# Kernel optimization log

Measured on AMD Instinct MI355X. Metric: run time of the kernel, lower is better.

## Reference

```python
import jax, jax.numpy as jnp
import numpy as np

M, N = 24, 12
H1 = (M + N) * 10 * 8        # 2880
HID = (M * M + N * N) * 10   # 7200
H2 = M * N * 4               # 1152
DOUT = M * N                 # 288
EPS = 1e-12


def setup_inputs() -> dict:
    key = jax.random.key(0)
    ks = jax.random.split(key, 16)
    s = 0.02  # weight scale
    return {
        "yt": jax.random.normal(ks[0], (N,), jnp.float32),
        "F": jax.random.normal(ks[1], (M, M), jnp.float32) * 0.1,
        "Hm": jax.random.normal(ks[2], (N, M), jnp.float32) * 0.1,
        "m1x_posterior": jax.random.normal(ks[3], (M, 1), jnp.float32),
        "m1x_prior_old": jax.random.normal(ks[4], (M, 1), jnp.float32),
        "hn": jax.random.normal(ks[5], (HID,), jnp.float32),
        "W1": jax.random.normal(ks[6], (H1, M + N), jnp.float32) * s,
        "b1": jax.random.normal(ks[7], (H1,), jnp.float32) * s,
        "Wih": jax.random.normal(ks[8], (3 * HID, H1), jnp.float32) * s,
        "Whh": jax.random.normal(ks[9], (3 * HID, HID), jnp.float32) * s,
        "bih": jax.random.normal(ks[10], (3 * HID,), jnp.float32) * s,
        "bhh": jax.random.normal(ks[11], (3 * HID,), jnp.float32) * s,
        "W2": jax.random.normal(ks[12], (H2, HID), jnp.float32) * s,
        "b2": jax.random.normal(ks[13], (H2,), jnp.float32) * s,
        "W3": jax.random.normal(ks[14], (DOUT, H2), jnp.float32) * s,
        "b3": jax.random.normal(ks[15], (DOUT,), jnp.float32) * s,
    }


def _l2_normalize(x):
    # torch F.normalize(p=2, dim=0, eps=1e-12)
    return x / jnp.maximum(jnp.linalg.norm(x), EPS)


def _gru_cell(x, h, Wih, Whh, bih, bhh):
    gi = Wih @ x + bih            # [3*HID]
    gh = Whh @ h + bhh            # [3*HID]
    gi_r, gi_z, gi_n = jnp.split(gi, 3)
    gh_r, gh_z, gh_n = jnp.split(gh, 3)
    r = jax.nn.sigmoid(gi_r + gh_r)
    z = jax.nn.sigmoid(gi_z + gh_z)
    n = jnp.tanh(gi_n + r * gh_n)
    return (1.0 - z) * n + z * h


def reference(yt, F, Hm, m1x_posterior, m1x_prior_old, hn,
              W1, b1, Wih, Whh, bih, bhh, W2, b2, W3, b3):
    # step_prior
    m1x_prior = F @ m1x_posterior        # [M,1]
    m1y = Hm @ m1x_prior                 # [N,1]
    # step_KGain_est
    dm1x = _l2_normalize((m1x_posterior - m1x_prior_old)[:, 0])  # [M]
    dm1y = _l2_normalize(yt - m1y[:, 0])                         # [N]
    kg_in = jnp.concatenate([dm1y, dm1x])                        # [M+N]
    l1 = jax.nn.relu(W1 @ kg_in + b1)                            # [H1]
    h_new = _gru_cell(l1, hn, Wih, Whh, bih, bhh)                # [HID]
    l2 = jax.nn.relu(W2 @ h_new + b2)                            # [H2]
    kg = (W3 @ l2 + b3).reshape(M, N)                            # Kalman gain
    # KNet_step update
    dy = yt[:, None] - m1y                                       # [N,1]
    m1x_post_new = m1x_prior + kg @ dy                           # [M,1]
    return m1x_post_new[:, 0]
```

## Files before the change

kernel.cpp:

```cpp
#include <hip/hip_runtime.h>
#include <math.h>

#define M_DIM 24
#define N_DIM 12
#define H1    2880
#define HID   7200
#define H2    1152
#define DOUT  288

#define WS_PRIOR 0
#define WS_KGIN  32
#define WS_DY    96
#define WS_L1    128
#define WS_HNEW  3072
#define WS_L2    10304
#define WS_KG    11520

__device__ __forceinline__ float wave_sum(float v) {
    #pragma unroll
    for (int o = 32; o; o >>= 1) v += __shfl_xor(v, o);
    return v;
}

__global__ void k_head(const float* __restrict__ yt, const float* __restrict__ F,
                       const float* __restrict__ Hm, const float* __restrict__ post,
                       const float* __restrict__ prior_old, float* __restrict__ ws) {
    __shared__ float s_prior[M_DIM];
    __shared__ float s_m1y[N_DIM];
    int t = threadIdx.x;
    if (t < M_DIM) {
        float acc = 0.f;
        #pragma unroll
        for (int j = 0; j < M_DIM; ++j) acc += F[t * M_DIM + j] * post[j];
        s_prior[t] = acc;
    }
    __syncthreads();
    if (t < N_DIM) {
        float acc = 0.f;
        #pragma unroll
        for (int j = 0; j < M_DIM; ++j) acc += Hm[t * M_DIM + j] * s_prior[j];
        s_m1y[t] = acc;
    }
    __syncthreads();
    float vx = 0.f;
    if (t < M_DIM) vx = post[t] - prior_old[t];
    float nx = fmaxf(sqrtf(wave_sum(vx * vx)), 1e-12f);
    float vy = 0.f;
    if (t < N_DIM) vy = yt[t] - s_m1y[t];
    float ny = fmaxf(sqrtf(wave_sum(vy * vy)), 1e-12f);
    if (t < N_DIM) ws[WS_KGIN + t] = vy / ny;
    if (t < M_DIM) ws[WS_KGIN + N_DIM + t] = vx / nx;
    if (t < M_DIM) ws[WS_PRIOR + t] = s_prior[t];
    if (t < N_DIM) ws[WS_DY + t] = vy;
}

__global__ __launch_bounds__(256) void k_l1(const float* __restrict__ W1,
                                            const float* __restrict__ b1,
                                            float* __restrict__ ws) {
    __shared__ float s_x[M_DIM + N_DIM];
    int t = threadIdx.x, lane = t & 63, w = t >> 6;
    if (t < M_DIM + N_DIM) s_x[t] = ws[WS_KGIN + t];
    __syncthreads();
    int i = blockIdx.x * 4 + w;
    float acc = (lane < M_DIM + N_DIM)
              ? W1[(size_t)i * (M_DIM + N_DIM) + lane] * s_x[lane] : 0.f;
    acc = wave_sum(acc);
    if (lane == 0) ws[WS_L1 + i] = fmaxf(acc + b1[i], 0.f);
}

__global__ __launch_bounds__(256) void k_gru(const float* __restrict__ Wih,
                                             const float* __restrict__ Whh,
                                             const float* __restrict__ bih,
                                             const float* __restrict__ bhh,
                                             const float* __restrict__ hn,
                                             float* __restrict__ ws) {
    __shared__ float s_l1[H1];
    __shared__ float s_h[HID];
    int t = threadIdx.x;
    float4* s_l14 = (float4*)s_l1;
    float4* s_h4  = (float4*)s_h;
    const float4* l14 = (const float4*)(ws + WS_L1);
    const float4* h4  = (const float4*)hn;
    for (int k = t; k < H1 / 4; k += 256)  s_l14[k] = l14[k];
    for (int k = t; k < HID / 4; k += 256) s_h4[k]  = h4[k];
    __syncthreads();

    int lane = t & 63, w = t >> 6;
    int i = blockIdx.x * 4 + w;

    const float4* wr = (const float4*)(Wih + (size_t)i * H1);
    const float4* wz = (const float4*)(Wih + (size_t)(i + HID) * H1);
    const float4* wn = (const float4*)(Wih + (size_t)(i + 2 * HID) * H1);
    float ar = 0.f, az = 0.f, an = 0.f;
    for (int k = lane; k < H1 / 4; k += 64) {
        float4 x = s_l14[k];
        float4 a = wr[k], b = wz[k], c = wn[k];
        ar += a.x * x.x + a.y * x.y + a.z * x.z + a.w * x.w;
        az += b.x * x.x + b.y * x.y + b.z * x.z + b.w * x.w;
        an += c.x * x.x + c.y * x.y + c.z * x.z + c.w * x.w;
    }

    const float4* ur = (const float4*)(Whh + (size_t)i * HID);
    const float4* uz = (const float4*)(Whh + (size_t)(i + HID) * HID);
    const float4* un = (const float4*)(Whh + (size_t)(i + 2 * HID) * HID);
    float hr = 0.f, hz = 0.f, hh = 0.f;
    for (int k = lane; k < HID / 4; k += 64) {
        float4 x = s_h4[k];
        float4 a = ur[k], b = uz[k], c = un[k];
        hr += a.x * x.x + a.y * x.y + a.z * x.z + a.w * x.w;
        hz += b.x * x.x + b.y * x.y + b.z * x.z + b.w * x.w;
        hh += c.x * x.x + c.y * x.y + c.z * x.z + c.w * x.w;
    }

    ar = wave_sum(ar); az = wave_sum(az); an = wave_sum(an);
    hr = wave_sum(hr); hz = wave_sum(hz); hh = wave_sum(hh);

    if (lane == 0) {
        float gr = ar + bih[i] + hr + bhh[i];
        float gz = az + bih[i + HID] + hz + bhh[i + HID];
        float r = 1.f / (1.f + expf(-gr));
        float z = 1.f / (1.f + expf(-gz));
        float n = tanhf(an + bih[i + 2 * HID] + r * (hh + bhh[i + 2 * HID]));
        ws[WS_HNEW + i] = (1.f - z) * n + z * s_h[i];
    }
}

__global__ __launch_bounds__(256) void k_l2(const float* __restrict__ W2,
                                            const float* __restrict__ b2,
                                            float* __restrict__ ws) {
    __shared__ float s_h[HID];
    int t = threadIdx.x;
    float4* s_h4 = (float4*)s_h;
    const float4* h4 = (const float4*)(ws + WS_HNEW);
    for (int k = t; k < HID / 4; k += 256) s_h4[k] = h4[k];
    __syncthreads();
    int lane = t & 63, w = t >> 6;
    int i = blockIdx.x * 4 + w;
    const float4* wr = (const float4*)(W2 + (size_t)i * HID);
    float acc = 0.f;
    for (int k = lane; k < HID / 4; k += 64) {
        float4 x = s_h4[k];
        float4 a = wr[k];
        acc += a.x * x.x + a.y * x.y + a.z * x.z + a.w * x.w;
    }
    acc = wave_sum(acc);
    if (lane == 0) ws[WS_L2 + i] = fmaxf(acc + b2[i], 0.f);
}

__global__ __launch_bounds__(256) void k_kg(const float* __restrict__ W3,
                                            const float* __restrict__ b3,
                                            float* __restrict__ ws) {
    __shared__ float s_x[H2];
    int t = threadIdx.x;
    float4* s_x4 = (float4*)s_x;
    const float4* x4 = (const float4*)(ws + WS_L2);
    for (int k = t; k < H2 / 4; k += 256) s_x4[k] = x4[k];
    __syncthreads();
    int lane = t & 63, w = t >> 6;
    int i = blockIdx.x * 4 + w;
    const float4* wr = (const float4*)(W3 + (size_t)i * H2);
    float acc = 0.f;
    for (int k = lane; k < H2 / 4; k += 64) {
        float4 x = s_x4[k];
        float4 a = wr[k];
        acc += a.x * x.x + a.y * x.y + a.z * x.z + a.w * x.w;
    }
    acc = wave_sum(acc);
    if (lane == 0) ws[WS_KG + i] = acc + b3[i];
}

__global__ void k_out(const float* __restrict__ ws, float* __restrict__ out) {
    int t = threadIdx.x;
    if (t < M_DIM) {
        float acc = ws[WS_PRIOR + t];
        #pragma unroll
        for (int n = 0; n < N_DIM; ++n)
            acc += ws[WS_KG + t * N_DIM + n] * ws[WS_DY + n];
        out[t] = acc;
    }
}

extern "C" void kernel_launch(void* const* d_in, const int* in_sizes, int n_in,
                              void* d_out, int out_size, void* d_ws, size_t ws_size,
                              hipStream_t stream) {
    const float* yt        = (const float*)d_in[0];
    const float* F         = (const float*)d_in[1];
    const float* Hm        = (const float*)d_in[2];
    const float* post      = (const float*)d_in[3];
    const float* prior_old = (const float*)d_in[4];
    const float* hn        = (const float*)d_in[5];
    const float* W1        = (const float*)d_in[6];
    const float* b1        = (const float*)d_in[7];
    const float* Wih       = (const float*)d_in[8];
    const float* Whh       = (const float*)d_in[9];
    const float* bih       = (const float*)d_in[10];
    const float* bhh       = (const float*)d_in[11];
    const float* W2        = (const float*)d_in[12];
    const float* b2        = (const float*)d_in[13];
    const float* W3        = (const float*)d_in[14];
    const float* b3        = (const float*)d_in[15];
    float* out = (float*)d_out;
    float* ws  = (float*)d_ws;

    k_head<<<1, 64, 0, stream>>>(yt, F, Hm, post, prior_old, ws);
    k_l1 <<<H1 / 4, 256, 0, stream>>>(W1, b1, ws);
    k_gru<<<HID / 4, 256, 0, stream>>>(Wih, Whh, bih, bhh, hn, ws);
    k_l2 <<<H2 / 4, 256, 0, stream>>>(W2, b2, ws);
    k_kg <<<DOUT / 4, 256, 0, stream>>>(W3, b3, ws);
    k_out<<<1, 64, 0, stream>>>(ws, out);
}
```

Measured before the change: 193.3 us.

## Fuse head into L1 and KG into output; drop shared-memory staging in GEMVs

The prior/normalization head is now recomputed redundantly in every L1 block, and the Kalman-gain GEMV is fused with the final update so each block produces one output row. This cuts the launch count from six to four. The GRU and L2 kernels no longer stage the input vector into shared memory; they read it straight from global memory, which should be served from cache. Those kernels also get occupancy hints and 2x unrolling. In exchange, the tiny head work is repeated in each of 720 blocks, and vector loads now go through the cache instead of LDS.

```diff
diff --git a/kernel.cpp b/kernel.cpp
--- a/kernel.cpp
+++ b/kernel.cpp
@@ -7,14 +7,13 @@
 #define HID   7200
 #define H2    1152
 #define DOUT  288
+#define KGIN  (M_DIM + N_DIM)
 
 #define WS_PRIOR 0
-#define WS_KGIN  32
 #define WS_DY    96
 #define WS_L1    128
 #define WS_HNEW  3072
 #define WS_L2    10304
-#define WS_KG    11520
 
 __device__ __forceinline__ float wave_sum(float v) {
     #pragma unroll
@@ -22,12 +21,18 @@
     return v;
 }
 
-__global__ void k_head(const float* __restrict__ yt, const float* __restrict__ F,
-                       const float* __restrict__ Hm, const float* __restrict__ post,
-                       const float* __restrict__ prior_old, float* __restrict__ ws) {
+__global__ __launch_bounds__(256) void k_l1h(
+        const float* __restrict__ yt, const float* __restrict__ F,
+        const float* __restrict__ Hm, const float* __restrict__ post,
+        const float* __restrict__ prior_old,
+        const float* __restrict__ W1, const float* __restrict__ b1,
+        float* __restrict__ ws) {
     __shared__ float s_prior[M_DIM];
     __shared__ float s_m1y[N_DIM];
-    int t = threadIdx.x;
+    __shared__ float s_x[KGIN];
+    __shared__ float s_dy[N_DIM];
+    int t = threadIdx.x, lane = t & 63, w = t >> 6;
+
     if (t < M_DIM) {
         float acc = 0.f;
         #pragma unroll
@@ -42,58 +47,46 @@
         s_m1y[t] = acc;
     }
     __syncthreads();
-    float vx = 0.f;
-    if (t < M_DIM) vx = post[t] - prior_old[t];
-    float nx = fmaxf(sqrtf(wave_sum(vx * vx)), 1e-12f);
-    float vy = 0.f;
-    if (t < N_DIM) vy = yt[t] - s_m1y[t];
-    float ny = fmaxf(sqrtf(wave_sum(vy * vy)), 1e-12f);
-    if (t < N_DIM) ws[WS_KGIN + t] = vy / ny;
-    if (t < M_DIM) ws[WS_KGIN + N_DIM + t] = vx / nx;
-    if (t < M_DIM) ws[WS_PRIOR + t] = s_prior[t];
-    if (t < N_DIM) ws[WS_DY + t] = vy;
-}
+    if (w == 0) {
+        float vx = 0.f;
+        if (lane < M_DIM) vx = post[lane] - prior_old[lane];
+        float nx = fmaxf(sqrtf(wave_sum(vx * vx)), 1e-12f);
+        float vy = 0.f;
+        if (lane < N_DIM) vy = yt[lane] - s_m1y[lane];
+        float ny = fmaxf(sqrtf(wave_sum(vy * vy)), 1e-12f);
+        if (lane < N_DIM) { s_x[lane] = vy / ny; s_dy[lane] = vy; }
+        if (lane < M_DIM) s_x[N_DIM + lane] = vx / nx;
+    }
+    __syncthreads();
 
-__global__ __launch_bounds__(256) void k_l1(const float* __restrict__ W1,
-                                            const float* __restrict__ b1,
-                                            float* __restrict__ ws) {
-    __shared__ float s_x[M_DIM + N_DIM];
-    int t = threadIdx.x, lane = t & 63, w = t >> 6;
-    if (t < M_DIM + N_DIM) s_x[t] = ws[WS_KGIN + t];
-    __syncthreads();
+    if (blockIdx.x == 0) {
+        if (t < M_DIM) ws[WS_PRIOR + t] = s_prior[t];
+        if (t < N_DIM) ws[WS_DY + t] = s_dy[t];
+    }
+
     int i = blockIdx.x * 4 + w;
-    float acc = (lane < M_DIM + N_DIM)
-              ? W1[(size_t)i * (M_DIM + N_DIM) + lane] * s_x[lane] : 0.f;
+    float acc = (lane < KGIN) ? W1[(size_t)i * KGIN + lane] * s_x[lane] : 0.f;
     acc = wave_sum(acc);
     if (lane == 0) ws[WS_L1 + i] = fmaxf(acc + b1[i], 0.f);
 }
 
-__global__ __launch_bounds__(256) void k_gru(const float* __restrict__ Wih,
-                                             const float* __restrict__ Whh,
-                                             const float* __restrict__ bih,
-                                             const float* __restrict__ bhh,
-                                             const float* __restrict__ hn,
-                                             float* __restrict__ ws) {
-    __shared__ float s_l1[H1];
-    __shared__ float s_h[HID];
-    int t = threadIdx.x;
-    float4* s_l14 = (float4*)s_l1;
-    float4* s_h4  = (float4*)s_h;
-    const float4* l14 = (const float4*)(ws + WS_L1);
-    const float4* h4  = (const float4*)hn;
-    for (int k = t; k < H1 / 4; k += 256)  s_l14[k] = l14[k];
-    for (int k = t; k < HID / 4; k += 256) s_h4[k]  = h4[k];
-    __syncthreads();
+__global__ __launch_bounds__(256, 4) void k_gru(
+        const float* __restrict__ Wih, const float* __restrict__ Whh,
+        const float* __restrict__ bih, const float* __restrict__ bhh,
+        const float* __restrict__ hn, float* __restrict__ ws) {
+    int t = threadIdx.x, lane = t & 63, w = t >> 6;
+    int i = blockIdx.x * 4 + w;
 
-    int lane = t & 63, w = t >> 6;
-    int i = blockIdx.x * 4 + w;
+    const float4* x1 = (const float4*)(ws + WS_L1);
+    const float4* xh = (const float4*)hn;
 
     const float4* wr = (const float4*)(Wih + (size_t)i * H1);
     const float4* wz = (const float4*)(Wih + (size_t)(i + HID) * H1);
     const float4* wn = (const float4*)(Wih + (size_t)(i + 2 * HID) * H1);
     float ar = 0.f, az = 0.f, an = 0.f;
+    #pragma unroll 2
     for (int k = lane; k < H1 / 4; k += 64) {
-        float4 x = s_l14[k];
+        float4 x = x1[k];
         float4 a = wr[k], b = wz[k], c = wn[k];
         ar += a.x * x.x + a.y * x.y + a.z * x.z + a.w * x.w;
         az += b.x * x.x + b.y * x.y + b.z * x.z + b.w * x.w;
@@ -104,8 +97,9 @@
     const float4* uz = (const float4*)(Whh + (size_t)(i + HID) * HID);
     const float4* un = (const float4*)(Whh + (size_t)(i + 2 * HID) * HID);
     float hr = 0.f, hz = 0.f, hh = 0.f;
+    #pragma unroll 2
     for (int k = lane; k < HID / 4; k += 64) {
-        float4 x = s_h4[k];
+        float4 x = xh[k];
         float4 a = ur[k], b = uz[k], c = un[k];
         hr += a.x * x.x + a.y * x.y + a.z * x.z + a.w * x.w;
         hz += b.x * x.x + b.y * x.y + b.z * x.z + b.w * x.w;
@@ -121,25 +115,21 @@
         float r = 1.f / (1.f + expf(-gr));
         float z = 1.f / (1.f + expf(-gz));
         float n = tanhf(an + bih[i + 2 * HID] + r * (hh + bhh[i + 2 * HID]));
-        ws[WS_HNEW + i] = (1.f - z) * n + z * s_h[i];
+        ws[WS_HNEW + i] = (1.f - z) * n + z * hn[i];
     }
 }
 
-__global__ __launch_bounds__(256) void k_l2(const float* __restrict__ W2,
-                                            const float* __restrict__ b2,
-                                            float* __restrict__ ws) {
-    __shared__ float s_h[HID];
-    int t = threadIdx.x;
-    float4* s_h4 = (float4*)s_h;
-    const float4* h4 = (const float4*)(ws + WS_HNEW);
-    for (int k = t; k < HID / 4; k += 256) s_h4[k] = h4[k];
-    __syncthreads();
-    int lane = t & 63, w = t >> 6;
+__global__ __launch_bounds__(256, 4) void k_l2(
+        const float* __restrict__ W2, const float* __restrict__ b2,
+        float* __restrict__ ws) {
+    int t = threadIdx.x, lane = t & 63, w = t >> 6;
     int i = blockIdx.x * 4 + w;
+    const float4* x4 = (const float4*)(ws + WS_HNEW);
     const float4* wr = (const float4*)(W2 + (size_t)i * HID);
     float acc = 0.f;
+    #pragma unroll 2
     for (int k = lane; k < HID / 4; k += 64) {
-        float4 x = s_h4[k];
+        float4 x = x4[k];
         float4 a = wr[k];
         acc += a.x * x.x + a.y * x.y + a.z * x.z + a.w * x.w;
     }
@@ -147,36 +137,29 @@
     if (lane == 0) ws[WS_L2 + i] = fmaxf(acc + b2[i], 0.f);
 }
 
-__global__ __launch_bounds__(256) void k_kg(const float* __restrict__ W3,
-                                            const float* __restrict__ b3,
-                                            float* __restrict__ ws) {
-    __shared__ float s_x[H2];
-    int t = threadIdx.x;
-    float4* s_x4 = (float4*)s_x;
+__global__ __launch_bounds__(768) void k_kg_out(
+        const float* __restrict__ W3, const float* __restrict__ b3,
+        const float* __restrict__ ws, float* __restrict__ out) {
+    __shared__ float s_kg[N_DIM];
+    int m = blockIdx.x;
+    int t = threadIdx.x, lane = t & 63, w = t >> 6;
+    int row = m * N_DIM + w;
+    const float4* wr = (const float4*)(W3 + (size_t)row * H2);
     const float4* x4 = (const float4*)(ws + WS_L2);
-    for (int k = t; k < H2 / 4; k += 256) s_x4[k] = x4[k];
-    __syncthreads();
-    int lane = t & 63, w = t >> 6;
-    int i = blockIdx.x * 4 + w;
-    const float4* wr = (const float4*)(W3 + (size_t)i * H2);
     float acc = 0.f;
     for (int k = lane; k < H2 / 4; k += 64) {
-        float4 x = s_x4[k];
+        float4 x = x4[k];
         float4 a = wr[k];
         acc += a.x * x.x + a.y * x.y + a.z * x.z + a.w * x.w;
     }
     acc = wave_sum(acc);
-    if (lane == 0) ws[WS_KG + i] = acc + b3[i];
-}
-
-__global__ void k_out(const float* __restrict__ ws, float* __restrict__ out) {
-    int t = threadIdx.x;
-    if (t < M_DIM) {
-        float acc = ws[WS_PRIOR + t];
+    if (lane == 0) s_kg[w] = acc + b3[row];
+    __syncthreads();
+    if (t == 0) {
+        float a = ws[WS_PRIOR + m];
         #pragma unroll
-        for (int n = 0; n < N_DIM; ++n)
-            acc += ws[WS_KG + t * N_DIM + n] * ws[WS_DY + n];
-        out[t] = acc;
+        for (int n = 0; n < N_DIM; ++n) a += s_kg[n] * ws[WS_DY + n];
+        out[m] = a;
     }
 }
 
@@ -202,10 +185,8 @@
     float* out = (float*)d_out;
     float* ws  = (float*)d_ws;
 
-    k_head<<<1, 64, 0, stream>>>(yt, F, Hm, post, prior_old, ws);
-    k_l1 <<<H1 / 4, 256, 0, stream>>>(W1, b1, ws);
-    k_gru<<<HID / 4, 256, 0, stream>>>(Wih, Whh, bih, bhh, hn, ws);
-    k_l2 <<<H2 / 4, 256, 0, stream>>>(W2, b2, ws);
-    k_kg <<<DOUT / 4, 256, 0, stream>>>(W3, b3, ws);
-    k_out<<<1, 64, 0, stream>>>(ws, out);
+    k_l1h  <<<H1 / 4, 256, 0, stream>>>(yt, F, Hm, post, prior_old, W1, b1, ws);
+    k_gru  <<<HID / 4, 256, 0, stream>>>(Wih, Whh, bih, bhh, hn, ws);
+    k_l2   <<<H2 / 4, 256, 0, stream>>>(W2, b2, ws);
+    k_kg_out<<<M_DIM, 768, 0, stream>>>(W3, b3, ws, out);
 }
```

Result: faster. 178.6 us (-7.6%).
